# Kernel optimization log

Measured on AMD Instinct MI355X. Metric: run time of the kernel, lower is better.

Reference implementation:

```python
import jax, jax.numpy as jnp
import numpy as np

NB_COMP, LAT_DIM, OUT_DIM, N = 16, 128, 512, 16384


def setup_inputs() -> dict:
    key = jax.random.key(0)
    ks = jax.random.split(key, 8)
    eps = jax.random.normal(ks[0], (N, LAT_DIM), dtype=jnp.float32)
    c = jax.random.randint(ks[1], (N,), 0, NB_COMP, dtype=jnp.int32)
    mu = jax.random.normal(ks[2], (NB_COMP, LAT_DIM), dtype=jnp.float32)
    sigma = jax.random.uniform(ks[3], (NB_COMP, LAT_DIM), dtype=jnp.float32)
    # Kaiming-ish init for the two expert linear layers
    W1 = jax.random.normal(ks[4], (NB_COMP, OUT_DIM, LAT_DIM), dtype=jnp.float32) / np.sqrt(LAT_DIM)
    b1 = jax.random.normal(ks[5], (NB_COMP, OUT_DIM), dtype=jnp.float32) * 0.01
    W2 = jax.random.normal(ks[6], (NB_COMP, OUT_DIM, OUT_DIM), dtype=jnp.float32) / np.sqrt(OUT_DIM)
    b2 = jax.random.normal(ks[7], (NB_COMP, OUT_DIM), dtype=jnp.float32) * 0.01
    return {"n": N, "eps": eps, "c": c, "mu": mu, "sigma": sigma,
            "W1": W1, "b1": b1, "W2": W2, "b2": b2}


def reference(n, eps, c, mu, sigma, W1, b1, W2, b2):
    # Per-sample latent from its component's mean-field variational dist:
    # lat[k] = eps[k] * sigma[c[k]] + mu[c[k]]
    lat = eps * sigma[c] + mu[c]                                  # (n, lat_dim)
    # Run every expert's 2-layer MLP densely, then select per-sample expert.
    hidden = jax.nn.relu(jnp.einsum("nd,chd->cnh", lat, W1) + b1[:, None, :])  # (C, n, H)
    out_all = jnp.einsum("cnh,cwh->cnw", hidden, W2) + b2[:, None, :]          # (C, n, W)
    return out_all[c, jnp.arange(n)]                              # (n, weights_dim)
```

## Files before the change

### kernel.cpp

```cpp
#include <hip/hip_runtime.h>

#define NB 16
#define LD 128
#define OD 512
#define NS 16384
#define NPMAX (NS + NB*128)
#define NMT (NPMAX/128)

typedef __attribute__((ext_vector_type(8))) short short8;
typedef __attribute__((ext_vector_type(4))) float f32x4;

#define WS_OFF     128
#define WS_POFF    256
#define WS_PERM    1024
#define WS_W1B     (128*1024)
#define WS_W2B     (WS_W1B + 2*1024*1024)
#define WS_HID     (WS_W2B + 8*1024*1024)

#define GLDS16(g, l) __builtin_amdgcn_global_load_lds( \
    (const __attribute__((address_space(1))) unsigned int*)(g), \
    (__attribute__((address_space(3))) unsigned int*)(l), 16, 0, 0)

static __device__ __forceinline__ unsigned short f2bf(float f) {
  unsigned int u = __float_as_uint(f);
  u += 0x7FFFu + ((u >> 16) & 1u);
  return (unsigned short)(u >> 16);
}

#define SORT_T 1024
#define SORT_CH (NS / SORT_T)
__global__ __launch_bounds__(SORT_T) void k_convsort(
    const float* __restrict__ W1, const float* __restrict__ W2,
    const int* __restrict__ c,
    unsigned short* __restrict__ W1b, unsigned short* __restrict__ W2b,
    int* __restrict__ off, int* __restrict__ poff, int* __restrict__ perm) {
  __shared__ int cnt[NB * SORT_T];
  __shared__ int totals[NB];
  __shared__ int ebase[NB];

  const int t = threadIdx.x;
  if (blockIdx.x == 0) {
    for (int e = 0; e < NB; ++e) cnt[e * SORT_T + t] = 0;
    __syncthreads();

    int myc[SORT_CH];
    for (int i = 0; i < SORT_CH; ++i) {
      int e = c[t * SORT_CH + i];
      myc[i] = e;
      cnt[e * SORT_T + t]++;
    }
    __syncthreads();

    const int w = t >> 6, l = t & 63;
    {
      int carry = 0;
      for (int chunk = 0; chunk < SORT_T / 64; ++chunk) {
        int idx = chunk * 64 + l;
        int v0 = cnt[w * SORT_T + idx];
        int v = v0;
        for (int d = 1; d < 64; d <<= 1) {
          int n = __shfl_up(v, d);
          if (l >= d) v += n;
        }
        cnt[w * SORT_T + idx] = carry + (v - v0);
        carry += __shfl(v, 63);
      }
      if (l == 0) totals[w] = carry;
    }
    __syncthreads();

    if (t == 0) {
      int o = 0, p = 0;
      for (int e = 0; e < NB; ++e) {
        off[e] = o; poff[e] = p; ebase[e] = o;
        o += totals[e];
        p += ((totals[e] + 127) >> 7) << 7;
      }
      off[NB] = o; poff[NB] = p;
    }
    __syncthreads();

    for (int i = 0; i < SORT_CH; ++i) {
      int e = myc[i];
      int pos = ebase[e] + cnt[e * SORT_T + t]++;
      perm[pos] = t * SORT_CH + i;
    }
  } else {
    const int n1 = NB * OD * LD / 4, n2 = NB * OD * OD / 4;
    for (int i = (blockIdx.x - 1) * SORT_T + t; i < n1 + n2;
         i += (gridDim.x - 1) * SORT_T) {
      float4 v; unsigned short* dst;
      if (i < n1) { v = ((const float4*)W1)[i]; dst = W1b + (size_t)i * 4; }
      else        { v = ((const float4*)W2)[i - n1]; dst = W2b + (size_t)(i - n1) * 4; }
      ushort4 o = make_ushort4(f2bf(v.x), f2bf(v.y), f2bf(v.z), f2bf(v.w));
      *(ushort4*)dst = o;
    }
  }
}

__global__ __launch_bounds__(256) void k_gemm1(
    const float* __restrict__ eps, const float* __restrict__ mu,
    const float* __restrict__ sigma, const float* __restrict__ b1,
    const unsigned short* __restrict__ W1b,
    const int* __restrict__ off, const int* __restrict__ poff,
    const int* __restrict__ perm, unsigned short* __restrict__ hidden) {
  __shared__ alignas(16) unsigned short As[128 * 64];
  __shared__ alignas(16) unsigned short Bs[128 * 64];
  __shared__ alignas(16) float s_sig[LD];
  __shared__ alignas(16) float s_mu[LD];

  const int L = blockIdx.x;
  const int s = (L & 7) * 72 + (L >> 3);
  const int mt = s >> 2, ct = s & 3;
  const int pr0 = mt * 128;
  if (pr0 >= poff[NB]) return;
  int e = 0;
  while (e < NB - 1 && poff[e + 1] <= pr0) e++;
  const int off_e = off[e];
  const int cnt   = off[e + 1] - off_e;
  const int l0    = pr0 - poff[e];

  const int t = threadIdx.x, w = t >> 6, lane = t & 63;
  const int wr = w >> 1, wc = w & 1;
  const int fr = lane & 15, fg = lane >> 4;
  const int srow = lane >> 3, scol = (lane & 7) * 8;

  if (t < LD) s_sig[t] = sigma[e * LD + t];
  else s_mu[t - LD] = mu[e * LD + (t - LD)];

  const int ar = t >> 1, ah = (t & 1) * 32;
  const int lrow = l0 + ar;
  const int asrc = (lrow < cnt) ? perm[off_e + lrow] : -1;
  __syncthreads();

  f32x4 acc[4][4] = {};
  for (int kt = 0; kt < 2; ++kt) {
#pragma unroll
    for (int i = 0; i < 4; ++i) {
      const int ci = w * 4 + i;
      const int row = ci * 8 + srow;
      GLDS16(W1b + ((size_t)e * OD + ct * 128 + row) * LD + kt * 64 + scol, Bs + ci * 512);
    }
    if (asrc >= 0) {
      const f32x4* ep = (const f32x4*)(eps + (size_t)asrc * LD + kt * 64 + ah);
      const f32x4* sg = (const f32x4*)(s_sig + kt * 64 + ah);
      const f32x4* mm = (const f32x4*)(s_mu + kt * 64 + ah);
#pragma unroll
      for (int j = 0; j < 4; ++j) {
        f32x4 v0 = ep[j * 2] * sg[j * 2] + mm[j * 2];
        f32x4 v1 = ep[j * 2 + 1] * sg[j * 2 + 1] + mm[j * 2 + 1];
        short8 o;
        o[0] = f2bf(v0[0]); o[1] = f2bf(v0[1]); o[2] = f2bf(v0[2]); o[3] = f2bf(v0[3]);
        o[4] = f2bf(v1[0]); o[5] = f2bf(v1[1]); o[6] = f2bf(v1[2]); o[7] = f2bf(v1[3]);
        *(short8*)(As + ar * 64 + ah + j * 8) = o;
      }
    } else {
      short8 z = {};
#pragma unroll
      for (int j = 0; j < 4; ++j) *(short8*)(As + ar * 64 + ah + j * 8) = z;
    }
    __syncthreads();
#pragma unroll
    for (int ks = 0; ks < 2; ++ks) {
      short8 a[4], b[4];
#pragma unroll
      for (int fm = 0; fm < 4; ++fm)
        a[fm] = *(const short8*)(As + (wr * 64 + fm * 16 + fr) * 64 + ks * 32 + fg * 8);
#pragma unroll
      for (int fn = 0; fn < 4; ++fn)
        b[fn] = *(const short8*)(Bs + (wc * 64 + fn * 16 + fr) * 64 + ks * 32 + fg * 8);
#pragma unroll
      for (int fm = 0; fm < 4; ++fm)
#pragma unroll
        for (int fn = 0; fn < 4; ++fn)
          acc[fm][fn] = __builtin_amdgcn_mfma_f32_16x16x32_bf16(a[fm], b[fn], acc[fm][fn], 0, 0, 0);
    }
    __syncthreads();
  }

  const int colb = ct * 128 + wc * 64;
  float bias[4];
#pragma unroll
  for (int fn = 0; fn < 4; ++fn) bias[fn] = b1[e * OD + colb + fn * 16 + fr];
#pragma unroll
  for (int fm = 0; fm < 4; ++fm) {
    const int row0 = pr0 + wr * 64 + fm * 16 + fg * 4;
#pragma unroll
    for (int j = 0; j < 4; ++j) {
      unsigned short* hrow = hidden + (size_t)(row0 + j) * OD + colb;
#pragma unroll
      for (int fn = 0; fn < 4; ++fn)
        hrow[fn * 16 + fr] = f2bf(fmaxf(acc[fm][fn][j] + bias[fn], 0.f));
    }
  }
}

__global__ __launch_bounds__(256) void k_gemm2(
    const float* __restrict__ b2, const unsigned short* __restrict__ W2b,
    const unsigned short* __restrict__ hidden,
    const int* __restrict__ off, const int* __restrict__ poff,
    const int* __restrict__ perm, float* __restrict__ out) {
  __shared__ alignas(16) unsigned short As[128 * 64];
  __shared__ alignas(16) unsigned short Bs[128 * 64];

  const int L = blockIdx.x;
  const int s = (L & 7) * 72 + (L >> 3);
  const int mt = s >> 2, ct = s & 3;
  const int pr0 = mt * 128;
  if (pr0 >= poff[NB]) return;
  int e = 0;
  while (e < NB - 1 && poff[e + 1] <= pr0) e++;
  const int off_e = off[e];
  const int cnt   = off[e + 1] - off_e;
  const int l0    = pr0 - poff[e];

  const int t = threadIdx.x, w = t >> 6, lane = t & 63;
  const int wr = w >> 1, wc = w & 1;
  const int fr = lane & 15, fg = lane >> 4;
  const int srow = lane >> 3, scol = (lane & 7) * 8;

  f32x4 acc[4][4] = {};
  for (int kt = 0; kt < 8; ++kt) {
#pragma unroll
    for (int i = 0; i < 4; ++i) {
      const int ci = w * 4 + i;
      const int row = ci * 8 + srow;
      GLDS16(hidden + (size_t)(pr0 + row) * OD + kt * 64 + scol, As + ci * 512);
      GLDS16(W2b + ((size_t)e * OD + ct * 128 + row) * OD + kt * 64 + scol, Bs + ci * 512);
    }
    __syncthreads();
#pragma unroll
    for (int ks = 0; ks < 2; ++ks) {
      short8 a[4], b[4];
#pragma unroll
      for (int fm = 0; fm < 4; ++fm)
        a[fm] = *(const short8*)(As + (wr * 64 + fm * 16 + fr) * 64 + ks * 32 + fg * 8);
#pragma unroll
      for (int fn = 0; fn < 4; ++fn)
        b[fn] = *(const short8*)(Bs + (wc * 64 + fn * 16 + fr) * 64 + ks * 32 + fg * 8);
#pragma unroll
      for (int fm = 0; fm < 4; ++fm)
#pragma unroll
        for (int fn = 0; fn < 4; ++fn)
          acc[fm][fn] = __builtin_amdgcn_mfma_f32_16x16x32_bf16(a[fm], b[fn], acc[fm][fn], 0, 0, 0);
    }
    __syncthreads();
  }

  const int colb = ct * 128 + wc * 64;
  float bias[4];
#pragma unroll
  for (int fn = 0; fn < 4; ++fn) bias[fn] = b2[e * OD + colb + fn * 16 + fr];
#pragma unroll
  for (int fm = 0; fm < 4; ++fm) {
    const int rl0 = wr * 64 + fm * 16 + fg * 4;
#pragma unroll
    for (int j = 0; j < 4; ++j) {
      const int lr = l0 + rl0 + j;
      if (lr < cnt) {
        const int k = perm[off_e + lr];
        float* orow = out + (size_t)k * OD + colb;
#pragma unroll
        for (int fn = 0; fn < 4; ++fn)
          orow[fn * 16 + fr] = acc[fm][fn][j] + bias[fn];
      }
    }
  }
}

extern "C" void kernel_launch(void* const* d_in, const int* in_sizes, int n_in,
                              void* d_out, int out_size, void* d_ws, size_t ws_size,
                              hipStream_t stream) {
  const float* eps   = (const float*)d_in[1];
  const int*   c     = (const int*)d_in[2];
  const float* mu    = (const float*)d_in[3];
  const float* sigma = (const float*)d_in[4];
  const float* W1    = (const float*)d_in[5];
  const float* b1    = (const float*)d_in[6];
  const float* W2    = (const float*)d_in[7];
  const float* b2    = (const float*)d_in[8];
  float* out = (float*)d_out;
  char*  ws  = (char*)d_ws;

  int* off     = (int*)(ws + WS_OFF);
  int* poff    = (int*)(ws + WS_POFF);
  int* perm    = (int*)(ws + WS_PERM);
  unsigned short* W1b = (unsigned short*)(ws + WS_W1B);
  unsigned short* W2b = (unsigned short*)(ws + WS_W2B);
  unsigned short* hid = (unsigned short*)(ws + WS_HID);

  k_convsort<<<512, SORT_T, 0, stream>>>(W1, W2, c, W1b, W2b, off, poff, perm);
  k_gemm1<<<576, 256, 0, stream>>>(eps, mu, sigma, b1, W1b, off, poff, perm, hid);
  k_gemm2<<<576, 256, 0, stream>>>(b2, W2b, hid, off, poff, perm, out);
}
```

Before: 69.07 us.

## Fuse both expert GEMMs into one kernel keeping hidden activations in LDS

Merges the two grouped GEMM kernels into one kernel. Each block owns a 64-row tile of sorted samples, computes the full 512-wide hidden layer into a swizzled 64KB LDS buffer, then runs the second GEMM from LDS. This drops the global round trip for the hidden tensor and one kernel launch. The cost is much larger LDS use per block, which lowers occupancy, plus a serial loop over output column chunks in each block. Each block now streams all of W1 and W2 for its expert, and only 288 blocks are launched.

```diff
diff --git a/kernel.cpp b/kernel.cpp
--- a/kernel.cpp
+++ b/kernel.cpp
@@ -5,7 +5,7 @@
 #define OD 512
 #define NS 16384
 #define NPMAX (NS + NB*128)
-#define NMT (NPMAX/128)
+#define NFB (NPMAX/64)
 
 typedef __attribute__((ext_vector_type(8))) short short8;
 typedef __attribute__((ext_vector_type(4))) float f32x4;
@@ -15,7 +15,6 @@
 #define WS_PERM    1024
 #define WS_W1B     (128*1024)
 #define WS_W2B     (WS_W1B + 2*1024*1024)
-#define WS_HID     (WS_W2B + 8*1024*1024)
 
 #define GLDS16(g, l) __builtin_amdgcn_global_load_lds( \
     (const __attribute__((address_space(1))) unsigned int*)(g), \
@@ -98,21 +97,19 @@
   }
 }
 
-__global__ __launch_bounds__(256) void k_gemm1(
+__global__ __launch_bounds__(256) void k_fused(
     const float* __restrict__ eps, const float* __restrict__ mu,
     const float* __restrict__ sigma, const float* __restrict__ b1,
-    const unsigned short* __restrict__ W1b,
+    const float* __restrict__ b2,
+    const unsigned short* __restrict__ W1b, const unsigned short* __restrict__ W2b,
     const int* __restrict__ off, const int* __restrict__ poff,
-    const int* __restrict__ perm, unsigned short* __restrict__ hidden) {
-  __shared__ alignas(16) unsigned short As[128 * 64];
-  __shared__ alignas(16) unsigned short Bs[128 * 64];
-  __shared__ alignas(16) float s_sig[LD];
-  __shared__ alignas(16) float s_mu[LD];
+    const int* __restrict__ perm, float* __restrict__ out) {
+  __shared__ alignas(16) unsigned short hid[64 * 512];
+  __shared__ alignas(16) unsigned short sb[8192];
 
   const int L = blockIdx.x;
-  const int s = (L & 7) * 72 + (L >> 3);
-  const int mt = s >> 2, ct = s & 3;
-  const int pr0 = mt * 128;
+  const int mt = (L & 7) * 36 + (L >> 3);
+  const int pr0 = mt * 64;
   if (pr0 >= poff[NB]) return;
   int e = 0;
   while (e < NB - 1 && poff[e + 1] <= pr0) e++;
@@ -121,149 +118,150 @@
   const int l0    = pr0 - poff[e];
 
   const int t = threadIdx.x, w = t >> 6, lane = t & 63;
-  const int wr = w >> 1, wc = w & 1;
+  const int wm = w >> 1, wn = w & 1;
   const int fr = lane & 15, fg = lane >> 4;
-  const int srow = lane >> 3, scol = (lane & 7) * 8;
-
-  if (t < LD) s_sig[t] = sigma[e * LD + t];
-  else s_mu[t - LD] = mu[e * LD + (t - LD)];
-
-  const int ar = t >> 1, ah = (t & 1) * 32;
-  const int lrow = l0 + ar;
-  const int asrc = (lrow < cnt) ? perm[off_e + lrow] : -1;
-  __syncthreads();
-
-  f32x4 acc[4][4] = {};
-  for (int kt = 0; kt < 2; ++kt) {
-#pragma unroll
-    for (int i = 0; i < 4; ++i) {
-      const int ci = w * 4 + i;
-      const int row = ci * 8 + srow;
-      GLDS16(W1b + ((size_t)e * OD + ct * 128 + row) * LD + kt * 64 + scol, Bs + ci * 512);
-    }
-    if (asrc >= 0) {
-      const f32x4* ep = (const f32x4*)(eps + (size_t)asrc * LD + kt * 64 + ah);
-      const f32x4* sg = (const f32x4*)(s_sig + kt * 64 + ah);
-      const f32x4* mm = (const f32x4*)(s_mu + kt * 64 + ah);
-#pragma unroll
-      for (int j = 0; j < 4; ++j) {
-        f32x4 v0 = ep[j * 2] * sg[j * 2] + mm[j * 2];
-        f32x4 v1 = ep[j * 2 + 1] * sg[j * 2 + 1] + mm[j * 2 + 1];
-        short8 o;
-        o[0] = f2bf(v0[0]); o[1] = f2bf(v0[1]); o[2] = f2bf(v0[2]); o[3] = f2bf(v0[3]);
-        o[4] = f2bf(v1[0]); o[5] = f2bf(v1[1]); o[6] = f2bf(v1[2]); o[7] = f2bf(v1[3]);
-        *(short8*)(As + ar * 64 + ah + j * 8) = o;
-      }
-    } else {
-      short8 z = {};
-#pragma unroll
-      for (int j = 0; j < 4; ++j) *(short8*)(As + ar * 64 + ah + j * 8) = z;
-    }
-    __syncthreads();
-#pragma unroll
-    for (int ks = 0; ks < 2; ++ks) {
-      short8 a[4], b[4];
-#pragma unroll
-      for (int fm = 0; fm < 4; ++fm)
-        a[fm] = *(const short8*)(As + (wr * 64 + fm * 16 + fr) * 64 + ks * 32 + fg * 8);
-#pragma unroll
-      for (int fn = 0; fn < 4; ++fn)
-        b[fn] = *(const short8*)(Bs + (wc * 64 + fn * 16 + fr) * 64 + ks * 32 + fg * 8);
-#pragma unroll
-      for (int fm = 0; fm < 4; ++fm)
-#pragma unroll
-        for (int fn = 0; fn < 4; ++fn)
-          acc[fm][fn] = __builtin_amdgcn_mfma_f32_16x16x32_bf16(a[fm], b[fn], acc[fm][fn], 0, 0, 0);
-    }
-    __syncthreads();
-  }
-
-  const int colb = ct * 128 + wc * 64;
-  float bias[4];
-#pragma unroll
-  for (int fn = 0; fn < 4; ++fn) bias[fn] = b1[e * OD + colb + fn * 16 + fr];
-#pragma unroll
-  for (int fm = 0; fm < 4; ++fm) {
-    const int row0 = pr0 + wr * 64 + fm * 16 + fg * 4;
+  const int slr = lane >> 3;
+  const int sinner = ((lane & 7) * 16) ^ ((slr & 7) << 4);
+
+  short8 a1[2][4];
+  int orow[2];
+  {
+    int lr0 = l0 + wm * 32 + fr;
+    orow[0] = (lr0 + 0  < cnt) ? perm[off_e + lr0] : -1;
+    orow[1] = (lr0 + 16 < cnt) ? perm[off_e + lr0 + 16] : -1;
+  }
+#pragma unroll
+  for (int q = 0; q < 4; ++q) {
+    const int k0 = q * 32 + fg * 8;
+    f32x4 s0 = *(const f32x4*)(sigma + e * LD + k0);
+    f32x4 s1 = *(const f32x4*)(sigma + e * LD + k0 + 4);
+    f32x4 m0 = *(const f32x4*)(mu + e * LD + k0);
+    f32x4 m1 = *(const f32x4*)(mu + e * LD + k0 + 4);
+#pragma unroll
+    for (int m = 0; m < 2; ++m) {
+      short8 o = {};
+      if (orow[m] >= 0) {
+        f32x4 e0 = *(const f32x4*)(eps + (size_t)orow[m] * LD + k0);
+        f32x4 e1 = *(const f32x4*)(eps + (size_t)orow[m] * LD + k0 + 4);
+        f32x4 v0 = e0 * s0 + m0, v1 = e1 * s1 + m1;
+        o[0] = (short)f2bf(v0[0]); o[1] = (short)f2bf(v0[1]);
+        o[2] = (short)f2bf(v0[2]); o[3] = (short)f2bf(v0[3]);
+        o[4] = (short)f2bf(v1[0]); o[5] = (short)f2bf(v1[1]);
+        o[6] = (short)f2bf(v1[2]); o[7] = (short)f2bf(v1[3]);
+      }
+      a1[m][q] = o;
+    }
+  }
+
+#pragma unroll 1
+  for (int nc = 0; nc < 4; ++nc) {
+    f32x4 acc1[2][4] = {};
+#pragma unroll
+    for (int kt1 = 0; kt1 < 2; ++kt1) {
+      __syncthreads();
+#pragma unroll
+      for (int i = 0; i < 4; ++i) {
+        const int seg = i * 4 + w;
+        const int row = seg * 8 + slr;
+        GLDS16((const char*)W1b + ((size_t)(e * OD + nc * 128 + row)) * 256
+                   + kt1 * 128 + sinner,
+               (char*)sb + seg * 1024);
+      }
+      __syncthreads();
+#pragma unroll
+      for (int ks = 0; ks < 2; ++ks) {
+        short8 b[4];
+#pragma unroll
+        for (int n = 0; n < 4; ++n) {
+          const int cl = wn * 64 + n * 16 + fr;
+          b[n] = *(const short8*)((const char*)sb + cl * 128 +
+                                  (((ks * 32 + fg * 8) * 2) ^ ((cl & 7) << 4)));
+        }
+#pragma unroll
+        for (int m = 0; m < 2; ++m)
+#pragma unroll
+          for (int n = 0; n < 4; ++n)
+            acc1[m][n] = __builtin_amdgcn_mfma_f32_16x16x32_bf16(
+                a1[m][kt1 * 2 + ks], b[n], acc1[m][n], 0, 0, 0);
+      }
+    }
+#pragma unroll
+    for (int n = 0; n < 4; ++n) {
+      const int col = nc * 128 + wn * 64 + n * 16 + fr;
+      const float bv = b1[e * OD + col];
+#pragma unroll
+      for (int m = 0; m < 2; ++m)
+#pragma unroll
+        for (int j = 0; j < 4; ++j) {
+          const int row = wm * 32 + m * 16 + fg * 4 + j;
+          const float v = fmaxf(acc1[m][n][j] + bv, 0.f);
+          *(unsigned short*)((char*)hid +
+              ((row * 1024 + col * 2) ^ ((row & 7) << 4))) = f2bf(v);
+        }
+    }
+  }
+
+  int kout[2][4];
+#pragma unroll
+  for (int m = 0; m < 2; ++m)
 #pragma unroll
     for (int j = 0; j < 4; ++j) {
-      unsigned short* hrow = hidden + (size_t)(row0 + j) * OD + colb;
-#pragma unroll
-      for (int fn = 0; fn < 4; ++fn)
-        hrow[fn * 16 + fr] = f2bf(fmaxf(acc[fm][fn][j] + bias[fn], 0.f));
-    }
-  }
-}
-
-__global__ __launch_bounds__(256) void k_gemm2(
-    const float* __restrict__ b2, const unsigned short* __restrict__ W2b,
-    const unsigned short* __restrict__ hidden,
-    const int* __restrict__ off, const int* __restrict__ poff,
-    const int* __restrict__ perm, float* __restrict__ out) {
-  __shared__ alignas(16) unsigned short As[128 * 64];
-  __shared__ alignas(16) unsigned short Bs[128 * 64];
-
-  const int L = blockIdx.x;
-  const int s = (L & 7) * 72 + (L >> 3);
-  const int mt = s >> 2, ct = s & 3;
-  const int pr0 = mt * 128;
-  if (pr0 >= poff[NB]) return;
-  int e = 0;
-  while (e < NB - 1 && poff[e + 1] <= pr0) e++;
-  const int off_e = off[e];
-  const int cnt   = off[e + 1] - off_e;
-  const int l0    = pr0 - poff[e];
-
-  const int t = threadIdx.x, w = t >> 6, lane = t & 63;
-  const int wr = w >> 1, wc = w & 1;
-  const int fr = lane & 15, fg = lane >> 4;
-  const int srow = lane >> 3, scol = (lane & 7) * 8;
-
-  f32x4 acc[4][4] = {};
-  for (int kt = 0; kt < 8; ++kt) {
-#pragma unroll
-    for (int i = 0; i < 4; ++i) {
-      const int ci = w * 4 + i;
-      const int row = ci * 8 + srow;
-      GLDS16(hidden + (size_t)(pr0 + row) * OD + kt * 64 + scol, As + ci * 512);
-      GLDS16(W2b + ((size_t)e * OD + ct * 128 + row) * OD + kt * 64 + scol, Bs + ci * 512);
-    }
-    __syncthreads();
-#pragma unroll
-    for (int ks = 0; ks < 2; ++ks) {
-      short8 a[4], b[4];
-#pragma unroll
-      for (int fm = 0; fm < 4; ++fm)
-        a[fm] = *(const short8*)(As + (wr * 64 + fm * 16 + fr) * 64 + ks * 32 + fg * 8);
-#pragma unroll
-      for (int fn = 0; fn < 4; ++fn)
-        b[fn] = *(const short8*)(Bs + (wc * 64 + fn * 16 + fr) * 64 + ks * 32 + fg * 8);
-#pragma unroll
-      for (int fm = 0; fm < 4; ++fm)
-#pragma unroll
-        for (int fn = 0; fn < 4; ++fn)
-          acc[fm][fn] = __builtin_amdgcn_mfma_f32_16x16x32_bf16(a[fm], b[fn], acc[fm][fn], 0, 0, 0);
-    }
-    __syncthreads();
-  }
-
-  const int colb = ct * 128 + wc * 64;
-  float bias[4];
-#pragma unroll
-  for (int fn = 0; fn < 4; ++fn) bias[fn] = b2[e * OD + colb + fn * 16 + fr];
-#pragma unroll
-  for (int fm = 0; fm < 4; ++fm) {
-    const int rl0 = wr * 64 + fm * 16 + fg * 4;
-#pragma unroll
-    for (int j = 0; j < 4; ++j) {
-      const int lr = l0 + rl0 + j;
-      if (lr < cnt) {
-        const int k = perm[off_e + lr];
-        float* orow = out + (size_t)k * OD + colb;
-#pragma unroll
-        for (int fn = 0; fn < 4; ++fn)
-          orow[fn * 16 + fr] = acc[fm][fn][j] + bias[fn];
-      }
+      const int lr = l0 + wm * 32 + m * 16 + fg * 4 + j;
+      kout[m][j] = (lr < cnt) ? perm[off_e + lr] : -1;
+    }
+
+#pragma unroll 1
+  for (int nc2 = 0; nc2 < 4; ++nc2) {
+    f32x4 acc2[2][4] = {};
+#pragma unroll 1
+    for (int kt = 0; kt < 8; ++kt) {
+      __syncthreads();
+#pragma unroll
+      for (int i = 0; i < 4; ++i) {
+        const int seg = i * 4 + w;
+        const int row = seg * 8 + slr;
+        GLDS16((const char*)W2b + ((size_t)(e * OD + nc2 * 128 + row)) * 1024
+                   + kt * 128 + sinner,
+               (char*)sb + seg * 1024);
+      }
+      short8 a2[2][2];
+#pragma unroll
+      for (int m = 0; m < 2; ++m)
+#pragma unroll
+        for (int ks = 0; ks < 2; ++ks) {
+          const int row = wm * 32 + m * 16 + fr;
+          const int kcol = kt * 64 + ks * 32 + fg * 8;
+          a2[m][ks] = *(const short8*)((const char*)hid +
+              ((row * 1024 + kcol * 2) ^ ((row & 7) << 4)));
+        }
+      __syncthreads();
+#pragma unroll
+      for (int ks = 0; ks < 2; ++ks) {
+        short8 b[4];
+#pragma unroll
+        for (int n = 0; n < 4; ++n) {
+          const int cl = wn * 64 + n * 16 + fr;
+          b[n] = *(const short8*)((const char*)sb + cl * 128 +
+                                  (((ks * 32 + fg * 8) * 2) ^ ((cl & 7) << 4)));
+        }
+#pragma unroll
+        for (int m = 0; m < 2; ++m)
+#pragma unroll
+          for (int n = 0; n < 4; ++n)
+            acc2[m][n] = __builtin_amdgcn_mfma_f32_16x16x32_bf16(
+                a2[m][ks], b[n], acc2[m][n], 0, 0, 0);
+      }
+    }
+#pragma unroll
+    for (int n = 0; n < 4; ++n) {
+      const int col = nc2 * 128 + wn * 64 + n * 16 + fr;
+      const float bv = b2[e * OD + col];
+#pragma unroll
+      for (int m = 0; m < 2; ++m)
+#pragma unroll
+        for (int j = 0; j < 4; ++j)
+          if (kout[m][j] >= 0)
+            out[(size_t)kout[m][j] * OD + col] = acc2[m][n][j] + bv;
     }
   }
 }
@@ -287,9 +285,8 @@
   int* perm    = (int*)(ws + WS_PERM);
   unsigned short* W1b = (unsigned short*)(ws + WS_W1B);
   unsigned short* W2b = (unsigned short*)(ws + WS_W2B);
-  unsigned short* hid = (unsigned short*)(ws + WS_HID);
 
   k_convsort<<<512, SORT_T, 0, stream>>>(W1, W2, c, W1b, W2b, off, poff, perm);
-  k_gemm1<<<576, 256, 0, stream>>>(eps, mu, sigma, b1, W1b, off, poff, perm, hid);
-  k_gemm2<<<576, 256, 0, stream>>>(b2, W2b, hid, off, poff, perm, out);
-}
+  k_fused<<<NFB, 256, 0, stream>>>(eps, mu, sigma, b1, b2, W1b, W2b,
+                                   off, poff, perm, out);
+}
```

Measured after the change: 77.11 us. +11.6%, slower.
